# Performance work log

Hardware: AMD Instinct MI355X
Metric: run time of the kernel (lower is better)

The kernel has to match this reference:

```python
import jax, jax.numpy as jnp
import numpy as np

N_FEATURES = 16384
N_EXPERTS = 8
D_IN = 768
EXPERT_DIM = N_FEATURES // N_EXPERTS  # 2048
N_TOKENS = 16384


def setup_inputs() -> dict:
    key = jax.random.key(0)
    k_act, k_preb, k_enc, k_dec, k_rb, k_r = jax.random.split(key, 6)
    activations = jax.random.normal(k_act, (N_TOKENS, D_IN), dtype=jnp.float32)
    pre_b = jax.random.normal(k_preb, (D_IN,), dtype=jnp.float32) * 0.01
    enc = jax.random.normal(k_enc, (N_EXPERTS, D_IN, EXPERT_DIM), dtype=jnp.float32) / (2.0 ** 0.5) / (D_IN ** 0.5)
    dec = jax.random.normal(k_dec, (N_EXPERTS, EXPERT_DIM, D_IN), dtype=jnp.float32) / (EXPERT_DIM ** 0.5)
    router_b = jax.random.normal(k_rb, (D_IN,), dtype=jnp.float32) * 0.01
    router = jax.random.normal(k_r, (D_IN, N_EXPERTS), dtype=jnp.float32) / (D_IN ** 0.5)
    return {"activations": activations, "pre_b": pre_b, "enc": enc, "dec": dec,
            "router_b": router_b, "router": router}


def reference(activations, pre_b, enc, dec, router_b, router):
    # Router: softmax over experts, top-1 routing.
    logits = (activations - router_b) @ router            # [N, E]
    probs = jax.nn.softmax(logits, axis=-1)
    expert_max_prob = jnp.max(probs, axis=-1)              # [N]
    expert_idx = jnp.argmax(probs, axis=-1)                # [N] int

    n_experts = enc.shape[0]
    recons = jnp.zeros_like(activations)
    # Fixed small loop over experts; tokens are masked (zeroed) per expert so
    # each per-expert encode/decode GEMM only contributes for its routed rows.
    for e in range(n_experts):
        mask = (expert_idx == e)[:, None]                  # [N, 1]
        x_e = jnp.where(mask, activations, 0.0)            # masked gather
        latent = jax.nn.relu(x_e @ enc[e])                 # [N, expert_dim]
        recon = latent @ dec[e]                            # [N, d_in]
        recons = recons + jnp.where(mask, recon, 0.0)      # scatter-combine

    return expert_max_prob[:, None] * recons + pre_b
```

## Files before the change

kernel.cpp:

```cpp
#include <hip/hip_runtime.h>
#include <hip/hip_bf16.h>
#include <hip/hip_fp16.h>

#define N_TOKENS 16384
#define D_IN 768
#define N_EXPERTS 8
#define EXPERT_DIM 2048

#define ROUTER_BLOCKS 256
#define TOK_PER_BLOCK 64

typedef _Float16 half8 __attribute__((ext_vector_type(8)));
typedef float floatx4 __attribute__((ext_vector_type(4)));

#define GBM 256
#define GBN 256
#define GBK 64

#define WAIT_VM0 0xF70

__device__ __forceinline__ void glds16(const _Float16* g, _Float16* l) {
    __builtin_amdgcn_global_load_lds(
        (const __attribute__((address_space(1))) unsigned int*)g,
        (__attribute__((address_space(3))) unsigned int*)l, 16, 0, 0);
}

__global__ __launch_bounds__(256) void convert_act(const float* __restrict__ act,
    _Float16* __restrict__ act_h)
{
    size_t i = ((size_t)blockIdx.x * 256 + threadIdx.x) * 8;
    float4 v0 = *(const float4*)(act + i);
    float4 v1 = *(const float4*)(act + i + 4);
    half8 h;
    h[0] = (_Float16)v0.x; h[1] = (_Float16)v0.y; h[2] = (_Float16)v0.z; h[3] = (_Float16)v0.w;
    h[4] = (_Float16)v1.x; h[5] = (_Float16)v1.y; h[6] = (_Float16)v1.z; h[7] = (_Float16)v1.w;
    *(half8*)(act_h + i) = h;
}

__global__ __launch_bounds__(256) void router_kernel(const float* __restrict__ act,
    const float* __restrict__ router_b, const float* __restrict__ router,
    float* __restrict__ prob, int* __restrict__ localpos, int* __restrict__ eidx,
    int* __restrict__ hist)
{
    __shared__ int h[N_EXPERTS];
    if (threadIdx.x < N_EXPERTS) h[threadIdx.x] = 0;
    __syncthreads();

    int wave = threadIdx.x >> 6, lane = threadIdx.x & 63;
#pragma unroll 1
    for (int it = 0; it < 16; ++it) {
        int t = blockIdx.x * TOK_PER_BLOCK + wave * 16 + it;
        float acc[8];
#pragma unroll
        for (int e = 0; e < 8; ++e) acc[e] = 0.f;
        const float* arow = act + (size_t)t * D_IN;
#pragma unroll
        for (int i0 = 0; i0 < D_IN; i0 += 64) {
            int i = i0 + lane;
            float a = arow[i] - router_b[i];
            const float* r = router + i * 8;
#pragma unroll
            for (int e = 0; e < 8; ++e) acc[e] += a * r[e];
        }
#pragma unroll
        for (int s = 32; s > 0; s >>= 1) {
#pragma unroll
            for (int e = 0; e < 8; ++e) acc[e] += __shfl_down(acc[e], s, 64);
        }
        if (lane == 0) {
            float m = acc[0]; int ai = 0;
#pragma unroll
            for (int e = 1; e < 8; ++e) if (acc[e] > m) { m = acc[e]; ai = e; }
            float s = 0.f;
#pragma unroll
            for (int e = 0; e < 8; ++e) s += __expf(acc[e] - m);
            prob[t] = 1.0f / s;
            eidx[t] = ai;
            localpos[t] = atomicAdd(&h[ai], 1);
        }
    }
    __syncthreads();
    if (threadIdx.x < N_EXPERTS) hist[blockIdx.x * N_EXPERTS + threadIdx.x] = h[threadIdx.x];
}

__global__ __launch_bounds__(256) void scan_kernel(int* __restrict__ hist,
    int* __restrict__ counts, int* __restrict__ offsets)
{
    __shared__ int sh[ROUTER_BLOCKS * N_EXPERTS];
    __shared__ int tot[N_EXPERTS], off[N_EXPERTS];
    int tid = threadIdx.x;
    *(int4*)&sh[tid * 8]     = *(const int4*)&hist[tid * 8];
    *(int4*)&sh[tid * 8 + 4] = *(const int4*)&hist[tid * 8 + 4];
    __syncthreads();
    if (tid < N_EXPERTS) {
        int run = 0;
        for (int b = 0; b < ROUTER_BLOCKS; ++b) {
            int v = sh[b * 8 + tid];
            sh[b * 8 + tid] = run;
            run += v;
        }
        tot[tid] = run;
    }
    __syncthreads();
    if (tid == 0) {
        int run = 0;
        for (int e = 0; e < N_EXPERTS; ++e) {
            off[e] = run; offsets[e] = run; counts[e] = tot[e]; run += tot[e];
        }
    }
    __syncthreads();
    int4 a = *(const int4*)&sh[tid * 8];
    int4 b = *(const int4*)&sh[tid * 8 + 4];
    a.x += off[0]; a.y += off[1]; a.z += off[2]; a.w += off[3];
    b.x += off[4]; b.y += off[5]; b.z += off[6]; b.w += off[7];
    *(int4*)&hist[tid * 8]     = a;
    *(int4*)&hist[tid * 8 + 4] = b;
}

__global__ __launch_bounds__(256) void order_kernel(const int* __restrict__ eidx,
    const int* __restrict__ localpos, const int* __restrict__ hist,
    int* __restrict__ order)
{
    int t = blockIdx.x * 256 + threadIdx.x;
    int base = hist[(t >> 6) * N_EXPERTS + eidx[t]];
    order[base + localpos[t]] = t;
}

__global__ __launch_bounds__(256) void transpose_to_half(const float* __restrict__ W,
    _Float16* __restrict__ WT, int K, int Nc)
{
    __shared__ _Float16 tile[64][72];
    size_t esz = (size_t)K * Nc;
    const float* We = W + (size_t)blockIdx.z * esz;
    _Float16* WTe = WT + (size_t)blockIdx.z * esz;
    int n0 = blockIdx.x * 64, k0 = blockIdx.y * 64;
    int tr = threadIdx.x >> 4;
    int tc = threadIdx.x & 15;
#pragma unroll
    for (int rr = 0; rr < 64; rr += 16) {
        int k = k0 + rr + tr;
        float4 v = *(const float4*)(We + (size_t)k * Nc + n0 + tc * 4);
        tile[tc * 4 + 0][rr + tr] = (_Float16)v.x;
        tile[tc * 4 + 1][rr + tr] = (_Float16)v.y;
        tile[tc * 4 + 2][rr + tr] = (_Float16)v.z;
        tile[tc * 4 + 3][rr + tr] = (_Float16)v.w;
    }
    __syncthreads();
#pragma unroll
    for (int p = 0; p < 2; ++p) {
        int id = threadIdx.x + p * 256;
        int r = id >> 3, ch = id & 7;
        half8 v = *(const half8*)&tile[r][ch * 8];
        *(half8*)(WTe + (size_t)(n0 + r) * K + k0 + ch * 8) = v;
    }
}

#define STAGE8(bufp, k0h)                                              \
    do {                                                               \
        glds16(pa0 + (k0h), (bufp) + 0 * 4096 + st_dst);               \
        glds16(pa1 + (k0h), (bufp) + 1 * 4096 + st_dst);               \
        glds16(pa2 + (k0h), (bufp) + 2 * 4096 + st_dst);               \
        glds16(pa3 + (k0h), (bufp) + 3 * 4096 + st_dst);               \
        glds16(pb0 + (k0h), (bufp) + 16384 + 0 * 4096 + st_dst);       \
        glds16(pb1 + (k0h), (bufp) + 16384 + 1 * 4096 + st_dst);       \
        glds16(pb2 + (k0h), (bufp) + 16384 + 2 * 4096 + st_dst);       \
        glds16(pb3 + (k0h), (bufp) + 16384 + 3 * 4096 + st_dst);       \
    } while (0)

__global__ __launch_bounds__(512, 2) void encode_kernel(const _Float16* __restrict__ act_h,
    const _Float16* __restrict__ encT, const int* __restrict__ order,
    const int* __restrict__ counts, const int* __restrict__ offsets,
    _Float16* __restrict__ latent)
{
    int id = blockIdx.x;
    int e = id & 7;
    int j = id >> 3;
    int nt = j & 7;
    int mt = j >> 3;

    int n_e = counts[e];
    if (mt * GBM >= n_e) return;
    int slot0 = offsets[e] + mt * GBM;
    int mrem = n_e - mt * GBM;

    __shared__ _Float16 lds[2][32768];
    __shared__ int s_tok[GBM];

    int tid = threadIdx.x;
    if (tid < GBM) s_tok[tid] = (tid < mrem) ? order[slot0 + tid] : order[slot0];
    __syncthreads();

    int w = tid >> 6, lane = tid & 63;
    int wm = w >> 2, wn = w & 3;
    int mrow = lane & 15;

    int st_dst = w * 512 + lane * 8;
    int c_st = ((lane & 7) - (w << 2) - (lane >> 4)) & 7;
    int row_st = w * 8 + (lane >> 3);
    const _Float16* Be = encT + (size_t)e * D_IN * EXPERT_DIM + (size_t)(nt * GBN) * D_IN;
    const _Float16* pa0 = act_h + (size_t)s_tok[0 * 64 + row_st] * D_IN + c_st * 8;
    const _Float16* pa1 = act_h + (size_t)s_tok[1 * 64 + row_st] * D_IN + c_st * 8;
    const _Float16* pa2 = act_h + (size_t)s_tok[2 * 64 + row_st] * D_IN + c_st * 8;
    const _Float16* pa3 = act_h + (size_t)s_tok[3 * 64 + row_st] * D_IN + c_st * 8;
    const _Float16* pb0 = Be + (size_t)(0 * 64 + row_st) * D_IN + c_st * 8;
    const _Float16* pb1 = Be + (size_t)(1 * 64 + row_st) * D_IN + c_st * 8;
    const _Float16* pb2 = Be + (size_t)(2 * 64 + row_st) * D_IN + c_st * 8;
    const _Float16* pb3 = Be + (size_t)(3 * 64 + row_st) * D_IN + c_st * 8;

    int c0 = ((lane >> 4) + (mrow >> 1)) & 7;
    int aoff0 = (wm * 128 + mrow) * 64 + c0 * 8;
    int aoff1 = (wm * 128 + mrow) * 64 + (c0 ^ 4) * 8;
    int boff0 = 16384 + (wn * 64 + mrow) * 64 + c0 * 8;
    int boff1 = 16384 + (wn * 64 + mrow) * 64 + (c0 ^ 4) * 8;

    floatx4 acc[8][4];
#pragma unroll
    for (int i = 0; i < 8; ++i)
#pragma unroll
        for (int jj = 0; jj < 4; ++jj) acc[i][jj] = (floatx4){0.f, 0.f, 0.f, 0.f};

    const int T = D_IN / GBK;
    STAGE8(&lds[0][0], 0);
    __builtin_amdgcn_s_waitcnt(WAIT_VM0);
    __builtin_amdgcn_s_barrier();

#pragma unroll 1
    for (int t = 0; t < T; ++t) {
        _Float16* cur = &lds[t & 1][0];
        if (t + 1 < T) {
            _Float16* nxt = &lds[(t + 1) & 1][0];
            int k1 = (t + 1) * GBK;
            STAGE8(nxt, k1);
        }
        half8 a0[8], b0[4];
#pragma unroll
        for (int i = 0; i < 8; ++i) a0[i] = *(const half8*)&cur[aoff0 + i * 1024];
#pragma unroll
        for (int jj = 0; jj < 4; ++jj) b0[jj] = *(const half8*)&cur[boff0 + jj * 1024];
        __builtin_amdgcn_s_setprio(1);
#pragma unroll
        for (int i = 0; i < 8; ++i)
#pragma unroll
            for (int jj = 0; jj < 4; ++jj)
                acc[i][jj] = __builtin_amdgcn_mfma_f32_16x16x32_f16(a0[i], b0[jj], acc[i][jj], 0, 0, 0);
        __builtin_amdgcn_s_setprio(0);
        half8 a1[8], b1[4];
#pragma unroll
        for (int i = 0; i < 8; ++i) a1[i] = *(const half8*)&cur[aoff1 + i * 1024];
#pragma unroll
        for (int jj = 0; jj < 4; ++jj) b1[jj] = *(const half8*)&cur[boff1 + jj * 1024];
        __builtin_amdgcn_s_setprio(1);
#pragma unroll
        for (int i = 0; i < 8; ++i)
#pragma unroll
            for (int jj = 0; jj < 4; ++jj)
                acc[i][jj] = __builtin_amdgcn_mfma_f32_16x16x32_f16(a1[i], b1[jj], acc[i][jj], 0, 0, 0);
        __builtin_amdgcn_s_setprio(0);
        if (t + 1 < T) {
            __builtin_amdgcn_s_waitcnt(WAIT_VM0);
            __builtin_amdgcn_s_barrier();
        }
    }

#pragma unroll
    for (int i = 0; i < 8; ++i) {
        int row0 = wm * 128 + i * 16 + (lane >> 4) * 4;
#pragma unroll
        for (int jj = 0; jj < 4; ++jj) {
            int col = nt * GBN + wn * 64 + jj * 16 + mrow;
#pragma unroll
            for (int r = 0; r < 4; ++r) {
                int row = row0 + r;
                if (row < mrem) {
                    float v = acc[i][jj][r];
                    v = v > 0.f ? v : 0.f;
                    latent[(size_t)(slot0 + row) * EXPERT_DIM + col] = (_Float16)v;
                }
            }
        }
    }
}

__global__ __launch_bounds__(512, 2) void decode_kernel(const _Float16* __restrict__ latent,
    const _Float16* __restrict__ decT, const int* __restrict__ order,
    const int* __restrict__ counts, const int* __restrict__ offsets,
    const float* __restrict__ prob, const float* __restrict__ pre_b,
    float* __restrict__ out)
{
    int id = blockIdx.x;
    int e = id & 7;
    int j = id >> 3;
    int nt = j % 3;
    int mt = j / 3;

    int n_e = counts[e];
    if (mt * GBM >= n_e) return;
    int slot0 = offsets[e] + mt * GBM;
    int mrem = n_e - mt * GBM;

    __shared__ _Float16 lds[2][32768];
    __shared__ int s_tok[GBM];
    __shared__ float s_p[GBM];

    int tid = threadIdx.x;
    if (tid < GBM) {
        int tok = (tid < mrem) ? order[slot0 + tid] : order[slot0];
        s_tok[tid] = tok;
        s_p[tid] = prob[tok];
    }
    __syncthreads();

    int w = tid >> 6, lane = tid & 63;
    int wm = w >> 2, wn = w & 3;
    int mrow = lane & 15;

    int st_dst = w * 512 + lane * 8;
    int c_st = ((lane & 7) - (w << 2) - (lane >> 4)) & 7;
    int row_st = w * 8 + (lane >> 3);
    const _Float16* Ae = latent + (size_t)slot0 * EXPERT_DIM;
    const _Float16* Be = decT + (size_t)e * EXPERT_DIM * D_IN + (size_t)(nt * GBN) * EXPERT_DIM;
    const _Float16* pa0 = Ae + (size_t)(0 * 64 + row_st) * EXPERT_DIM + c_st * 8;
    const _Float16* pa1 = Ae + (size_t)(1 * 64 + row_st) * EXPERT_DIM + c_st * 8;
    const _Float16* pa2 = Ae + (size_t)(2 * 64 + row_st) * EXPERT_DIM + c_st * 8;
    const _Float16* pa3 = Ae + (size_t)(3 * 64 + row_st) * EXPERT_DIM + c_st * 8;
    const _Float16* pb0 = Be + (size_t)(0 * 64 + row_st) * EXPERT_DIM + c_st * 8;
    const _Float16* pb1 = Be + (size_t)(1 * 64 + row_st) * EXPERT_DIM + c_st * 8;
    const _Float16* pb2 = Be + (size_t)(2 * 64 + row_st) * EXPERT_DIM + c_st * 8;
    const _Float16* pb3 = Be + (size_t)(3 * 64 + row_st) * EXPERT_DIM + c_st * 8;

    int c0 = ((lane >> 4) + (mrow >> 1)) & 7;
    int aoff0 = (wm * 128 + mrow) * 64 + c0 * 8;
    int aoff1 = (wm * 128 + mrow) * 64 + (c0 ^ 4) * 8;
    int boff0 = 16384 + (wn * 64 + mrow) * 64 + c0 * 8;
    int boff1 = 16384 + (wn * 64 + mrow) * 64 + (c0 ^ 4) * 8;

    floatx4 acc[8][4];
#pragma unroll
    for (int i = 0; i < 8; ++i)
#pragma unroll
        for (int jj = 0; jj < 4; ++jj) acc[i][jj] = (floatx4){0.f, 0.f, 0.f, 0.f};

    const int T = EXPERT_DIM / GBK;
    STAGE8(&lds[0][0], 0);
    __builtin_amdgcn_s_waitcnt(WAIT_VM0);
    __builtin_amdgcn_s_barrier();

#pragma unroll 1
    for (int t = 0; t < T; ++t) {
        _Float16* cur = &lds[t & 1][0];
        if (t + 1 < T) {
            _Float16* nxt = &lds[(t + 1) & 1][0];
            int k1 = (t + 1) * GBK;
            STAGE8(nxt, k1);
        }
        half8 a0[8], b0[4];
#pragma unroll
        for (int i = 0; i < 8; ++i) a0[i] = *(const half8*)&cur[aoff0 + i * 1024];
#pragma unroll
        for (int jj = 0; jj < 4; ++jj) b0[jj] = *(const half8*)&cur[boff0 + jj * 1024];
        __builtin_amdgcn_s_setprio(1);
#pragma unroll
        for (int i = 0; i < 8; ++i)
#pragma unroll
            for (int jj = 0; jj < 4; ++jj)
                acc[i][jj] = __builtin_amdgcn_mfma_f32_16x16x32_f16(a0[i], b0[jj], acc[i][jj], 0, 0, 0);
        __builtin_amdgcn_s_setprio(0);
        half8 a1[8], b1[4];
#pragma unroll
        for (int i = 0; i < 8; ++i) a1[i] = *(const half8*)&cur[aoff1 + i * 1024];
#pragma unroll
        for (int jj = 0; jj < 4; ++jj) b1[jj] = *(const half8*)&cur[boff1 + jj * 1024];
        __builtin_amdgcn_s_setprio(1);
#pragma unroll
        for (int i = 0; i < 8; ++i)
#pragma unroll
            for (int jj = 0; jj < 4; ++jj)
                acc[i][jj] = __builtin_amdgcn_mfma_f32_16x16x32_f16(a1[i], b1[jj], acc[i][jj], 0, 0, 0);
        __builtin_amdgcn_s_setprio(0);
        if (t + 1 < T) {
            __builtin_amdgcn_s_waitcnt(WAIT_VM0);
            __builtin_amdgcn_s_barrier();
        }
    }

#pragma unroll
    for (int i = 0; i < 8; ++i) {
        int row0 = wm * 128 + i * 16 + (lane >> 4) * 4;
#pragma unroll
        for (int jj = 0; jj < 4; ++jj) {
            int col = nt * GBN + wn * 64 + jj * 16 + mrow;
            float pb = pre_b[col];
#pragma unroll
            for (int r = 0; r < 4; ++r) {
                int row = row0 + r;
                if (row < mrem) {
                    out[(size_t)s_tok[row] * D_IN + col] = s_p[row] * acc[i][jj][r] + pb;
                }
            }
        }
    }
}

extern "C" void kernel_launch(void* const* d_in, const int* in_sizes, int n_in,
                              void* d_out, int out_size, void* d_ws, size_t ws_size,
                              hipStream_t stream)
{
    const float* act      = (const float*)d_in[0];
    const float* pre_b    = (const float*)d_in[1];
    const float* enc      = (const float*)d_in[2];
    const float* dec      = (const float*)d_in[3];
    const float* router_b = (const float*)d_in[4];
    const float* router   = (const float*)d_in[5];
    float* out = (float*)d_out;

    char* w = (char*)d_ws;
    int* counts  = (int*)w;  w += 256;
    int* offsets = (int*)w;  w += 256;
    int* hist    = (int*)w;  w += ROUTER_BLOCKS * N_EXPERTS * 4;
    int* eidx    = (int*)w;  w += N_TOKENS * 4;
    int* lpos    = (int*)w;  w += N_TOKENS * 4;
    int* order   = (int*)w;  w += N_TOKENS * 4;
    float* prob  = (float*)w; w += N_TOKENS * 4;
    _Float16* act_h  = (_Float16*)w; w += (size_t)N_TOKENS * D_IN * 2;
    _Float16* encT   = (_Float16*)w; w += (size_t)N_EXPERTS * D_IN * EXPERT_DIM * 2;
    _Float16* decT   = (_Float16*)w; w += (size_t)N_EXPERTS * D_IN * EXPERT_DIM * 2;
    _Float16* latent = (_Float16*)w; w += (size_t)(N_TOKENS + GBM) * EXPERT_DIM * 2;

    router_kernel<<<ROUTER_BLOCKS, 256, 0, stream>>>(act, router_b, router, prob, lpos, eidx, hist);
    scan_kernel<<<1, 256, 0, stream>>>(hist, counts, offsets);
    order_kernel<<<N_TOKENS / 256, 256, 0, stream>>>(eidx, lpos, hist, order);

    convert_act<<<N_TOKENS * D_IN / (256 * 8), 256, 0, stream>>>(act, act_h);
    transpose_to_half<<<dim3(EXPERT_DIM / 64, D_IN / 64, N_EXPERTS), 256, 0, stream>>>(enc, encT, D_IN, EXPERT_DIM);
    transpose_to_half<<<dim3(D_IN / 64, EXPERT_DIM / 64, N_EXPERTS), 256, 0, stream>>>(dec, decT, EXPERT_DIM, D_IN);

    encode_kernel<<<4096, 512, 0, stream>>>(act_h, encT, order, counts, offsets, latent);
    decode_kernel<<<1536, 512, 0, stream>>>(latent, decT, order, counts, offsets, prob, pre_b, out);
}
```

Before: 385.0 us.

## Fuse fp16 conversion into router, retile decode to 192 columns, change LDS swizzle

Merges the activation fp32-to-fp16 conversion into the router kernel so activations are read once, with vectorized float4 loads and router_b hoisted into registers. Retiles the decode GEMM from 256-wide to 192-wide N tiles (4 N tiles instead of 3), which launches more blocks and uses less LDS and fewer accumulator registers per block. Changes the LDS swizzle pattern in both encode and decode. The risks are lower per-block arithmetic intensity in decode and possible bank conflicts if the new swizzle is worse.

```diff
diff --git a/kernel.cpp b/kernel.cpp
--- a/kernel.cpp
+++ b/kernel.cpp
@@ -11,10 +11,10 @@
 #define TOK_PER_BLOCK 64
 
 typedef _Float16 half8 __attribute__((ext_vector_type(8)));
+typedef _Float16 half4 __attribute__((ext_vector_type(4)));
 typedef float floatx4 __attribute__((ext_vector_type(4)));
 
 #define GBM 256
-#define GBN 256
 #define GBK 64
 
 #define WAIT_VM0 0xF70
@@ -25,42 +25,47 @@
         (__attribute__((address_space(3))) unsigned int*)l, 16, 0, 0);
 }
 
-__global__ __launch_bounds__(256) void convert_act(const float* __restrict__ act,
-    _Float16* __restrict__ act_h)
-{
-    size_t i = ((size_t)blockIdx.x * 256 + threadIdx.x) * 8;
-    float4 v0 = *(const float4*)(act + i);
-    float4 v1 = *(const float4*)(act + i + 4);
-    half8 h;
-    h[0] = (_Float16)v0.x; h[1] = (_Float16)v0.y; h[2] = (_Float16)v0.z; h[3] = (_Float16)v0.w;
-    h[4] = (_Float16)v1.x; h[5] = (_Float16)v1.y; h[6] = (_Float16)v1.z; h[7] = (_Float16)v1.w;
-    *(half8*)(act_h + i) = h;
-}
-
-__global__ __launch_bounds__(256) void router_kernel(const float* __restrict__ act,
+__global__ __launch_bounds__(256) void router_convert(const float* __restrict__ act,
     const float* __restrict__ router_b, const float* __restrict__ router,
-    float* __restrict__ prob, int* __restrict__ localpos, int* __restrict__ eidx,
-    int* __restrict__ hist)
+    _Float16* __restrict__ act_h, float* __restrict__ prob, int* __restrict__ localpos,
+    int* __restrict__ eidx, int* __restrict__ hist)
 {
     __shared__ int h[N_EXPERTS];
     if (threadIdx.x < N_EXPERTS) h[threadIdx.x] = 0;
     __syncthreads();
 
     int wave = threadIdx.x >> 6, lane = threadIdx.x & 63;
+
+    float rb[3][4];
+#pragma unroll
+    for (int c = 0; c < 3; ++c) {
+        float4 v = *(const float4*)(router_b + lane * 4 + c * 256);
+        rb[c][0] = v.x; rb[c][1] = v.y; rb[c][2] = v.z; rb[c][3] = v.w;
+    }
+
 #pragma unroll 1
     for (int it = 0; it < 16; ++it) {
         int t = blockIdx.x * TOK_PER_BLOCK + wave * 16 + it;
+        const float* arow = act + (size_t)t * D_IN;
         float acc[8];
 #pragma unroll
         for (int e = 0; e < 8; ++e) acc[e] = 0.f;
-        const float* arow = act + (size_t)t * D_IN;
-#pragma unroll
-        for (int i0 = 0; i0 < D_IN; i0 += 64) {
-            int i = i0 + lane;
-            float a = arow[i] - router_b[i];
-            const float* r = router + i * 8;
-#pragma unroll
-            for (int e = 0; e < 8; ++e) acc[e] += a * r[e];
+#pragma unroll
+        for (int c = 0; c < 3; ++c) {
+            int i0 = lane * 4 + c * 256;
+            float4 v = *(const float4*)(arow + i0);
+            half4 hv;
+            hv[0] = (_Float16)v.x; hv[1] = (_Float16)v.y;
+            hv[2] = (_Float16)v.z; hv[3] = (_Float16)v.w;
+            *(half4*)(act_h + (size_t)t * D_IN + i0) = hv;
+            float va[4] = {v.x, v.y, v.z, v.w};
+#pragma unroll
+            for (int q = 0; q < 4; ++q) {
+                float a = va[q] - rb[c][q];
+                const float* r = router + (size_t)(i0 + q) * 8;
+#pragma unroll
+                for (int e = 0; e < 8; ++e) acc[e] += a * r[e];
+            }
         }
 #pragma unroll
         for (int s = 32; s > 0; s >>= 1) {
@@ -155,7 +160,53 @@
     }
 }
 
-#define STAGE8(bufp, k0h)                                              \
+__global__ __launch_bounds__(512, 2) void encode_kernel(const _Float16* __restrict__ act_h,
+    const _Float16* __restrict__ encT, const int* __restrict__ order,
+    const int* __restrict__ counts, const int* __restrict__ offsets,
+    _Float16* __restrict__ latent)
+{
+    int id = blockIdx.x;
+    int e = id & 7;
+    int j = id >> 3;
+    int nt = j & 7;
+    int mt = j >> 3;
+
+    int n_e = counts[e];
+    if (mt * GBM >= n_e) return;
+    int slot0 = offsets[e] + mt * GBM;
+    int mrem = n_e - mt * GBM;
+
+    __shared__ _Float16 lds[2][32768];
+    __shared__ int s_tok[GBM];
+
+    int tid = threadIdx.x;
+    if (tid < GBM) s_tok[tid] = (tid < mrem) ? order[slot0 + tid] : order[slot0];
+    __syncthreads();
+
+    int w = tid >> 6, lane = tid & 63;
+    int wm = w >> 2, wn = w & 3;
+    int mrow = lane & 15;
+
+    int st_dst = w * 512 + lane * 8;
+    int c_st = ((lane & 7) - (lane >> 3)) & 7;
+    int row_st = w * 8 + (lane >> 3);
+    const _Float16* Be = encT + (size_t)e * D_IN * EXPERT_DIM + (size_t)(nt * 256) * D_IN;
+    const _Float16* pa0 = act_h + (size_t)s_tok[0 * 64 + row_st] * D_IN + c_st * 8;
+    const _Float16* pa1 = act_h + (size_t)s_tok[1 * 64 + row_st] * D_IN + c_st * 8;
+    const _Float16* pa2 = act_h + (size_t)s_tok[2 * 64 + row_st] * D_IN + c_st * 8;
+    const _Float16* pa3 = act_h + (size_t)s_tok[3 * 64 + row_st] * D_IN + c_st * 8;
+    const _Float16* pb0 = Be + (size_t)(0 * 64 + row_st) * D_IN + c_st * 8;
+    const _Float16* pb1 = Be + (size_t)(1 * 64 + row_st) * D_IN + c_st * 8;
+    const _Float16* pb2 = Be + (size_t)(2 * 64 + row_st) * D_IN + c_st * 8;
+    const _Float16* pb3 = Be + (size_t)(3 * 64 + row_st) * D_IN + c_st * 8;
+
+    int c0 = ((lane >> 4) + (lane & 7)) & 7;
+    int aoff0 = (wm * 128 + mrow) * 64 + c0 * 8;
+    int aoff1 = (wm * 128 + mrow) * 64 + (c0 ^ 4) * 8;
+    int boff0 = 16384 + (wn * 64 + mrow) * 64 + c0 * 8;
+    int boff1 = 16384 + (wn * 64 + mrow) * 64 + (c0 ^ 4) * 8;
+
+#define ENC_STAGE(bufp, k0h)                                           \
     do {                                                               \
         glds16(pa0 + (k0h), (bufp) + 0 * 4096 + st_dst);               \
         glds16(pa1 + (k0h), (bufp) + 1 * 4096 + st_dst);               \
@@ -167,52 +218,6 @@
         glds16(pb3 + (k0h), (bufp) + 16384 + 3 * 4096 + st_dst);       \
     } while (0)
 
-__global__ __launch_bounds__(512, 2) void encode_kernel(const _Float16* __restrict__ act_h,
-    const _Float16* __restrict__ encT, const int* __restrict__ order,
-    const int* __restrict__ counts, const int* __restrict__ offsets,
-    _Float16* __restrict__ latent)
-{
-    int id = blockIdx.x;
-    int e = id & 7;
-    int j = id >> 3;
-    int nt = j & 7;
-    int mt = j >> 3;
-
-    int n_e = counts[e];
-    if (mt * GBM >= n_e) return;
-    int slot0 = offsets[e] + mt * GBM;
-    int mrem = n_e - mt * GBM;
-
-    __shared__ _Float16 lds[2][32768];
-    __shared__ int s_tok[GBM];
-
-    int tid = threadIdx.x;
-    if (tid < GBM) s_tok[tid] = (tid < mrem) ? order[slot0 + tid] : order[slot0];
-    __syncthreads();
-
-    int w = tid >> 6, lane = tid & 63;
-    int wm = w >> 2, wn = w & 3;
-    int mrow = lane & 15;
-
-    int st_dst = w * 512 + lane * 8;
-    int c_st = ((lane & 7) - (w << 2) - (lane >> 4)) & 7;
-    int row_st = w * 8 + (lane >> 3);
-    const _Float16* Be = encT + (size_t)e * D_IN * EXPERT_DIM + (size_t)(nt * GBN) * D_IN;
-    const _Float16* pa0 = act_h + (size_t)s_tok[0 * 64 + row_st] * D_IN + c_st * 8;
-    const _Float16* pa1 = act_h + (size_t)s_tok[1 * 64 + row_st] * D_IN + c_st * 8;
-    const _Float16* pa2 = act_h + (size_t)s_tok[2 * 64 + row_st] * D_IN + c_st * 8;
-    const _Float16* pa3 = act_h + (size_t)s_tok[3 * 64 + row_st] * D_IN + c_st * 8;
-    const _Float16* pb0 = Be + (size_t)(0 * 64 + row_st) * D_IN + c_st * 8;
-    const _Float16* pb1 = Be + (size_t)(1 * 64 + row_st) * D_IN + c_st * 8;
-    const _Float16* pb2 = Be + (size_t)(2 * 64 + row_st) * D_IN + c_st * 8;
-    const _Float16* pb3 = Be + (size_t)(3 * 64 + row_st) * D_IN + c_st * 8;
-
-    int c0 = ((lane >> 4) + (mrow >> 1)) & 7;
-    int aoff0 = (wm * 128 + mrow) * 64 + c0 * 8;
-    int aoff1 = (wm * 128 + mrow) * 64 + (c0 ^ 4) * 8;
-    int boff0 = 16384 + (wn * 64 + mrow) * 64 + c0 * 8;
-    int boff1 = 16384 + (wn * 64 + mrow) * 64 + (c0 ^ 4) * 8;
-
     floatx4 acc[8][4];
 #pragma unroll
     for (int i = 0; i < 8; ++i)
@@ -220,7 +225,7 @@
         for (int jj = 0; jj < 4; ++jj) acc[i][jj] = (floatx4){0.f, 0.f, 0.f, 0.f};
 
     const int T = D_IN / GBK;
-    STAGE8(&lds[0][0], 0);
+    ENC_STAGE(&lds[0][0], 0);
     __builtin_amdgcn_s_waitcnt(WAIT_VM0);
     __builtin_amdgcn_s_barrier();
 
@@ -229,8 +234,7 @@
         _Float16* cur = &lds[t & 1][0];
         if (t + 1 < T) {
             _Float16* nxt = &lds[(t + 1) & 1][0];
-            int k1 = (t + 1) * GBK;
-            STAGE8(nxt, k1);
+            ENC_STAGE(nxt, (t + 1) * GBK);
         }
         half8 a0[8], b0[4];
 #pragma unroll
@@ -261,13 +265,14 @@
             __builtin_amdgcn_s_barrier();
         }
     }
+#undef ENC_STAGE
 
 #pragma unroll
     for (int i = 0; i < 8; ++i) {
         int row0 = wm * 128 + i * 16 + (lane >> 4) * 4;
 #pragma unroll
         for (int jj = 0; jj < 4; ++jj) {
-            int col = nt * GBN + wn * 64 + jj * 16 + mrow;
+            int col = nt * 256 + wn * 64 + jj * 16 + mrow;
 #pragma unroll
             for (int r = 0; r < 4; ++r) {
                 int row = row0 + r;
@@ -290,15 +295,15 @@
     int id = blockIdx.x;
     int e = id & 7;
     int j = id >> 3;
-    int nt = j % 3;
-    int mt = j / 3;
+    int nt = j & 3;
+    int mt = j >> 2;
 
     int n_e = counts[e];
     if (mt * GBM >= n_e) return;
     int slot0 = offsets[e] + mt * GBM;
     int mrem = n_e - mt * GBM;
 
-    __shared__ _Float16 lds[2][32768];
+    __shared__ _Float16 lds[2][28672];
     __shared__ int s_tok[GBM];
     __shared__ float s_p[GBM];
 
@@ -315,10 +320,10 @@
     int mrow = lane & 15;
 
     int st_dst = w * 512 + lane * 8;
-    int c_st = ((lane & 7) - (w << 2) - (lane >> 4)) & 7;
+    int c_st = ((lane & 7) - (lane >> 3)) & 7;
     int row_st = w * 8 + (lane >> 3);
     const _Float16* Ae = latent + (size_t)slot0 * EXPERT_DIM;
-    const _Float16* Be = decT + (size_t)e * EXPERT_DIM * D_IN + (size_t)(nt * GBN) * EXPERT_DIM;
+    const _Float16* Be = decT + (size_t)e * EXPERT_DIM * D_IN + (size_t)(nt * 192) * EXPERT_DIM;
     const _Float16* pa0 = Ae + (size_t)(0 * 64 + row_st) * EXPERT_DIM + c_st * 8;
     const _Float16* pa1 = Ae + (size_t)(1 * 64 + row_st) * EXPERT_DIM + c_st * 8;
     const _Float16* pa2 = Ae + (size_t)(2 * 64 + row_st) * EXPERT_DIM + c_st * 8;
@@ -326,22 +331,32 @@
     const _Float16* pb0 = Be + (size_t)(0 * 64 + row_st) * EXPERT_DIM + c_st * 8;
     const _Float16* pb1 = Be + (size_t)(1 * 64 + row_st) * EXPERT_DIM + c_st * 8;
     const _Float16* pb2 = Be + (size_t)(2 * 64 + row_st) * EXPERT_DIM + c_st * 8;
-    const _Float16* pb3 = Be + (size_t)(3 * 64 + row_st) * EXPERT_DIM + c_st * 8;
-
-    int c0 = ((lane >> 4) + (mrow >> 1)) & 7;
+
+    int c0 = ((lane >> 4) + (lane & 7)) & 7;
     int aoff0 = (wm * 128 + mrow) * 64 + c0 * 8;
     int aoff1 = (wm * 128 + mrow) * 64 + (c0 ^ 4) * 8;
-    int boff0 = 16384 + (wn * 64 + mrow) * 64 + c0 * 8;
-    int boff1 = 16384 + (wn * 64 + mrow) * 64 + (c0 ^ 4) * 8;
-
-    floatx4 acc[8][4];
+    int boff0 = 16384 + (wn * 48 + mrow) * 64 + c0 * 8;
+    int boff1 = 16384 + (wn * 48 + mrow) * 64 + (c0 ^ 4) * 8;
+
+#define DEC_STAGE(bufp, k0h)                                           \
+    do {                                                               \
+        glds16(pa0 + (k0h), (bufp) + 0 * 4096 + st_dst);               \
+        glds16(pa1 + (k0h), (bufp) + 1 * 4096 + st_dst);               \
+        glds16(pa2 + (k0h), (bufp) + 2 * 4096 + st_dst);               \
+        glds16(pa3 + (k0h), (bufp) + 3 * 4096 + st_dst);               \
+        glds16(pb0 + (k0h), (bufp) + 16384 + 0 * 4096 + st_dst);       \
+        glds16(pb1 + (k0h), (bufp) + 16384 + 1 * 4096 + st_dst);       \
+        glds16(pb2 + (k0h), (bufp) + 16384 + 2 * 4096 + st_dst);       \
+    } while (0)
+
+    floatx4 acc[8][3];
 #pragma unroll
     for (int i = 0; i < 8; ++i)
 #pragma unroll
-        for (int jj = 0; jj < 4; ++jj) acc[i][jj] = (floatx4){0.f, 0.f, 0.f, 0.f};
+        for (int jj = 0; jj < 3; ++jj) acc[i][jj] = (floatx4){0.f, 0.f, 0.f, 0.f};
 
     const int T = EXPERT_DIM / GBK;
-    STAGE8(&lds[0][0], 0);
+    DEC_STAGE(&lds[0][0], 0);
     __builtin_amdgcn_s_waitcnt(WAIT_VM0);
     __builtin_amdgcn_s_barrier();
 
@@ -350,31 +365,30 @@
         _Float16* cur = &lds[t & 1][0];
         if (t + 1 < T) {
             _Float16* nxt = &lds[(t + 1) & 1][0];
-            int k1 = (t + 1) * GBK;
-            STAGE8(nxt, k1);
-        }
-        half8 a0[8], b0[4];
+            DEC_STAGE(nxt, (t + 1) * GBK);
+        }
+        half8 a0[8], b0[3];
 #pragma unroll
         for (int i = 0; i < 8; ++i) a0[i] = *(const half8*)&cur[aoff0 + i * 1024];
 #pragma unroll
-        for (int jj = 0; jj < 4; ++jj) b0[jj] = *(const half8*)&cur[boff0 + jj * 1024];
+        for (int jj = 0; jj < 3; ++jj) b0[jj] = *(const half8*)&cur[boff0 + jj * 1024];
         __builtin_amdgcn_s_setprio(1);
 #pragma unroll
         for (int i = 0; i < 8; ++i)
 #pragma unroll
-            for (int jj = 0; jj < 4; ++jj)
+            for (int jj = 0; jj < 3; ++jj)
                 acc[i][jj] = __builtin_amdgcn_mfma_f32_16x16x32_f16(a0[i], b0[jj], acc[i][jj], 0, 0, 0);
         __builtin_amdgcn_s_setprio(0);
-        half8 a1[8], b1[4];
+        half8 a1[8], b1[3];
 #pragma unroll
         for (int i = 0; i < 8; ++i) a1[i] = *(const half8*)&cur[aoff1 + i * 1024];
 #pragma unroll
-        for (int jj = 0; jj < 4; ++jj) b1[jj] = *(const half8*)&cur[boff1 + jj * 1024];
+        for (int jj = 0; jj < 3; ++jj) b1[jj] = *(const half8*)&cur[boff1 + jj * 1024];
         __builtin_amdgcn_s_setprio(1);
 #pragma unroll
         for (int i = 0; i < 8; ++i)
 #pragma unroll
-            for (int jj = 0; jj < 4; ++jj)
+            for (int jj = 0; jj < 3; ++jj)
                 acc[i][jj] = __builtin_amdgcn_mfma_f32_16x16x32_f16(a1[i], b1[jj], acc[i][jj], 0, 0, 0);
         __builtin_amdgcn_s_setprio(0);
         if (t + 1 < T) {
@@ -382,13 +396,14 @@
             __builtin_amdgcn_s_barrier();
         }
     }
+#undef DEC_STAGE
 
 #pragma unroll
     for (int i = 0; i < 8; ++i) {
         int row0 = wm * 128 + i * 16 + (lane >> 4) * 4;
 #pragma unroll
-        for (int jj = 0; jj < 4; ++jj) {
-            int col = nt * GBN + wn * 64 + jj * 16 + mrow;
+        for (int jj = 0; jj < 3; ++jj) {
+            int col = nt * 192 + wn * 48 + jj * 16 + mrow;
             float pb = pre_b[col];
 #pragma unroll
             for (int r = 0; r < 4; ++r) {
@@ -426,14 +441,13 @@
     _Float16* decT   = (_Float16*)w; w += (size_t)N_EXPERTS * D_IN * EXPERT_DIM * 2;
     _Float16* latent = (_Float16*)w; w += (size_t)(N_TOKENS + GBM) * EXPERT_DIM * 2;
 
-    router_kernel<<<ROUTER_BLOCKS, 256, 0, stream>>>(act, router_b, router, prob, lpos, eidx, hist);
+    router_convert<<<ROUTER_BLOCKS, 256, 0, stream>>>(act, router_b, router, act_h, prob, lpos, eidx, hist);
     scan_kernel<<<1, 256, 0, stream>>>(hist, counts, offsets);
     order_kernel<<<N_TOKENS / 256, 256, 0, stream>>>(eidx, lpos, hist, order);
 
-    convert_act<<<N_TOKENS * D_IN / (256 * 8), 256, 0, stream>>>(act, act_h);
     transpose_to_half<<<dim3(EXPERT_DIM / 64, D_IN / 64, N_EXPERTS), 256, 0, stream>>>(enc, encT, D_IN, EXPERT_DIM);
     transpose_to_half<<<dim3(D_IN / 64, EXPERT_DIM / 64, N_EXPERTS), 256, 0, stream>>>(dec, decT, EXPERT_DIM, D_IN);
 
     encode_kernel<<<4096, 512, 0, stream>>>(act_h, encT, order, counts, offsets, latent);
-    decode_kernel<<<1536, 512, 0, stream>>>(latent, decT, order, counts, offsets, prob, pre_b, out);
-}
+    decode_kernel<<<2048, 512, 0, stream>>>(latent, decT, order, counts, offsets, prob, pre_b, out);
+}
```

Result: slower. 403.2 us (+4.7%).
